# Optimization experiments

Measured on AMD Instinct MI355X. Metric: run time of the kernel, lower is better.

Reference implementation:

```python
import jax, jax.numpy as jnp
import numpy as np

TREE_DEPTH = 8
N_INTERNAL = 2 ** TREE_DEPTH - 1   # 255
N_LEAVES = 2 ** TREE_DEPTH         # 256
N_CLASSES = 100
N_TREES = 16
BATCH = 8192
D_FEAT = 1024
TEMPERATURE = 1.0


def setup_inputs() -> dict:
    key = jax.random.key(0)
    k1, k2, k3, k4, k5 = jax.random.split(key, 5)
    x = jax.random.normal(k1, (BATCH, D_FEAT), dtype=jnp.float32)
    # scale weights ~1/sqrt(D) so split logits are O(1) (avoids sigmoid saturation)
    split_weights = jax.random.normal(k2, (N_TREES, N_INTERNAL, D_FEAT), dtype=jnp.float32) / np.sqrt(D_FEAT)
    split_bias = jax.random.normal(k3, (N_TREES, N_INTERNAL), dtype=jnp.float32)
    leaf_logits = jax.random.normal(k4, (N_TREES, N_LEAVES, N_CLASSES), dtype=jnp.float32)
    tree_weights = jax.random.normal(k5, (N_TREES,), dtype=jnp.float32)
    return {"x": x, "split_weights": split_weights, "split_bias": split_bias,
            "leaf_logits": leaf_logits, "tree_weights": tree_weights}


def reference(x, split_weights, split_bias, leaf_logits, tree_weights):
    # All internal-node split logits in one contraction: [T, B, N_INTERNAL]
    logits = jnp.einsum('bd,tnd->tbn', x, split_weights) + split_bias[:, None, :]
    split_prob = jax.nn.sigmoid(logits / TEMPERATURE)  # P(go right) per heap node
    T, B = split_prob.shape[0], split_prob.shape[1]
    # Level-order path products. Heap layout: level d occupies nodes [2^d-1, 2^(d+1)-2].
    # Child j of a node splits into (left=2j, right=2j+1) at next level -> interleave.
    mu = jnp.ones((T, B, 1), dtype=x.dtype)
    for d in range(TREE_DEPTH):
        start = 2 ** d - 1
        p = split_prob[:, :, start:start + 2 ** d]          # [T, B, 2^d]
        mu = jnp.stack([mu * (1.0 - p), mu * p], axis=-1)   # left, right
        mu = mu.reshape(T, B, 2 ** (d + 1))
    # mu: [T, B, N_LEAVES] leaf reach probabilities, ordering matches leaf_idx
    leaf_dist = jax.nn.softmax(leaf_logits, axis=-1)        # [T, L, C]
    per_tree = jnp.einsum('tbl,tlc->tbc', mu, leaf_dist)    # [T, B, C]
    w = jax.nn.softmax(tree_weights, axis=0)[:, None, None]
    return (per_tree * w).sum(axis=0)                       # [B, C]
```

## Files before the change

kernel.cpp:

```cpp
#include <hip/hip_runtime.h>
#include <hip/hip_fp16.h>

typedef _Float16 f16;
typedef _Float16 f16x4 __attribute__((ext_vector_type(4)));
typedef _Float16 f16x8 __attribute__((ext_vector_type(8)));
typedef float    f32x4 __attribute__((ext_vector_type(4)));

constexpr int TREES = 16;
constexpr int NNODE = 255;
constexpr int NCLS  = 100;
constexpr int NCPAD = 112;
constexpr int NB    = 8192;
constexpr int DF    = 1024;
constexpr int KTOT  = TREES * 256;

constexpr size_t XH_OFF = 0;
constexpr size_t WH_OFF = XH_OFF + (size_t)NB * DF;
constexpr size_t SD_OFF = WH_OFF + (size_t)TREES * 256 * DF;
constexpr size_t BP_OFF = SD_OFF + (size_t)NCPAD * KTOT;
constexpr size_t PT_OFF_F = (BP_OFF + 8192) / 2;

#define WAIT_VMCNT(n) asm volatile("s_waitcnt vmcnt(" #n ")" ::: "memory")
__device__ __forceinline__ void BAR() {
  asm volatile("" ::: "memory");
  __builtin_amdgcn_s_barrier();
  asm volatile("" ::: "memory");
}

__device__ __forceinline__ void gload_lds16(const f16* g, f16* l) {
  __builtin_amdgcn_global_load_lds(
      (const __attribute__((address_space(1))) void*)g,
      (__attribute__((address_space(3))) void*)l, 16, 0, 0);
}

__global__ void prep_all_k(const float* __restrict__ x, const float* __restrict__ w,
                           const float* __restrict__ ll, const float* __restrict__ twin,
                           const float* __restrict__ sb,
                           f16* __restrict__ xh, f16* __restrict__ wh,
                           f16* __restrict__ sdt, float* __restrict__ bp) {
  int bid = blockIdx.x;
  if (bid < 4096) {
    int i = bid * 256 + threadIdx.x;
    const float4* s = (const float4*)x + (size_t)i * 2;
    float4 u = s[0], v = s[1];
    f16x8 h = {(f16)u.x, (f16)u.y, (f16)u.z, (f16)u.w,
               (f16)v.x, (f16)v.y, (f16)v.z, (f16)v.w};
    *((f16x8*)xh + i) = h;
  } else if (bid < 6144) {
    int i = (bid - 4096) * 256 + threadIdx.x;
    int flat = i * 8;
    int t = flat >> 18;
    int r = (flat >> 10) & 255;
    int k = flat & 1023;
    f16x8 h;
    if (r < NNODE) {
      const float4* s = (const float4*)(w + ((size_t)(t * NNODE + r) * DF + k));
      float4 u = s[0], v = s[1];
      h = (f16x8){(f16)u.x, (f16)u.y, (f16)u.z, (f16)u.w,
                  (f16)v.x, (f16)v.y, (f16)v.z, (f16)v.w};
    } else {
      h = (f16x8){(f16)0.f, (f16)0.f, (f16)0.f, (f16)0.f,
                  (f16)0.f, (f16)0.f, (f16)0.f, (f16)0.f};
    }
    *((f16x8*)wh + i) = h;
  } else {
    int wv   = threadIdx.x >> 6;
    int lane = threadIdx.x & 63;
    int id   = (bid - 6144) * 4 + wv;
    int t    = id >> 8;
    int node = id & 255;

    float wm = -1e30f;
#pragma unroll
    for (int i = 0; i < 16; ++i) wm = fmaxf(wm, twin[i]);
    float wsum = 0.f;
#pragma unroll
    for (int i = 0; i < 16; ++i) wsum += __expf(twin[i] - wm);
    float wt = __expf(twin[t] - wm) / wsum;

    const float* rowp = ll + (size_t)id * NCLS;
    float v1 = rowp[lane];
    bool has2 = (lane + 64) < NCLS;
    float v2 = has2 ? rowp[lane + 64] : -1e30f;
    float mx = fmaxf(v1, v2);
#pragma unroll
    for (int m = 32; m; m >>= 1) mx = fmaxf(mx, __shfl_xor(mx, m, 64));
    float e1 = __expf(v1 - mx);
    float e2 = has2 ? __expf(v2 - mx) : 0.f;
    float ss = e1 + e2;
#pragma unroll
    for (int m = 32; m; m >>= 1) ss += __shfl_xor(ss, m, 64);
    float inv = wt / ss;

    sdt[(size_t)lane * KTOT + id] = (f16)(e1 * inv);
    if (lane + 64 < NCPAD)
      sdt[(size_t)(lane + 64) * KTOT + id] = has2 ? (f16)(e2 * inv) : (f16)0.f;
    if (lane == 0) bp[id] = (node < NNODE) ? sb[(size_t)t * NNODE + node] : 0.f;
  }
}

__global__ __launch_bounds__(512, 2) void tree_gemm1(
    const f16* __restrict__ xh, const f16* __restrict__ wh,
    const float* __restrict__ biasp, const f16* __restrict__ sdt,
    float* __restrict__ ptree) {
  __shared__ f16 smem[81920];
  char* smb = (char*)smem;

  const int tid  = threadIdx.x;
  const int lane = tid & 63;
  const int wid  = tid >> 6;
  const int l15  = lane & 15;
  const int lq   = lane >> 4;
  const int wrow = (wid >> 2) * 128;
  const int wcol = (wid & 3) * 64;

  int bid  = blockIdx.x;
  int xcd  = bid & 7;
  int idx  = bid >> 3;
  int t    = (xcd & 1) * 8 + (idx & 7);
  int brow = (xcd >> 1) * 8 + (idx >> 3);

  const f16* xsrc = xh + (size_t)brow * 256 * DF;
  const f16* wsrc = wh + (size_t)t * 256 * DF;

  auto stage_ht = [&](int kt, int cb, int op, int kh) {
    const f16* srcb = (op == 0 ? xsrc : wsrc) + kt * 64 + kh * 32;
    f16* dstb = smem + cb * 32768 + op * 16384 + kh * 8192;
#pragma unroll
    for (int ch = 0; ch < 2; ++ch) {
      int u  = ch * 512 + tid;
      int r0 = ((u >> 2) ^ (u >> 4)) & 1;
      int r1 = (u >> 3) & 1;
      int r2 = (u >> 4) & 1;
      int r  = r0 | (r1 << 1) | (r2 << 2) | ((u >> 5) << 3);
      int cs = ((u ^ r0) & 1) | ((((u >> 1) ^ r1) & 1) << 1);
      gload_lds16(srcb + (size_t)r * DF + cs * 8, dstb + u * 8);
    }
  };

  auto sdt_stage2 = [&](int c) {
#pragma unroll
    for (int ch = 0; ch < 2; ++ch) {
      int q  = c * 1024 + ch * 512 + tid;
      int rr = q >> 5;
      int jj = q & 31;
      gload_lds16(sdt + (size_t)rr * KTOT + t * 256 + ((jj * 8) ^ ((rr & 7) << 3)),
                  smem + q * 8);
    }
  };

  auto ldop = [&](const char* half_base, int row) -> f16x8 {
    return *(const f16x8*)(half_base + ((row * 64 + lq * 16) ^ ((row & 7) << 4)));
  };

  f32x4 acc[8][4];
#pragma unroll
  for (int m = 0; m < 8; ++m)
#pragma unroll
    for (int n = 0; n < 4; ++n) acc[m][n] = (f32x4){0.f, 0.f, 0.f, 0.f};

  stage_ht(0, 0, 0, 0); stage_ht(0, 0, 1, 0);
  stage_ht(0, 0, 0, 1); stage_ht(0, 0, 1, 1);

  for (int kt = 0; kt < 16; ++kt) {
    const char* Acur = smb + (kt & 1) * 65536;
    const char* Bcur = Acur + 32768;
    const int cn = (kt & 1) ^ 1;
    f16x8 af[4], bf[4];

    if (kt < 15) stage_ht(kt + 1, cn, 0, 0); else sdt_stage2(0);
    WAIT_VMCNT(6);
    BAR();
#pragma unroll
    for (int m = 0; m < 4; ++m) af[m] = ldop(Acur, wrow + m * 16 + l15);
#pragma unroll
    for (int n = 0; n < 4; ++n) bf[n] = ldop(Bcur, wcol + n * 16 + l15);
    __builtin_amdgcn_s_setprio(1);
#pragma unroll
    for (int m = 0; m < 4; ++m)
#pragma unroll
      for (int n = 0; n < 4; ++n)
        acc[m][n] = __builtin_amdgcn_mfma_f32_16x16x32_f16(bf[n], af[m], acc[m][n], 0, 0, 0);
    __builtin_amdgcn_s_setprio(0);
    BAR();

#pragma unroll
    for (int m = 0; m < 4; ++m) af[m] = ldop(Acur, wrow + 64 + m * 16 + l15);
    if (kt < 15) stage_ht(kt + 1, cn, 1, 0);
    BAR();
    __builtin_amdgcn_sched_barrier(0);
    __builtin_amdgcn_s_setprio(1);
#pragma unroll
    for (int m = 0; m < 4; ++m)
#pragma unroll
      for (int n = 0; n < 4; ++n)
        acc[m + 4][n] = __builtin_amdgcn_mfma_f32_16x16x32_f16(bf[n], af[m], acc[m + 4][n], 0, 0, 0);
    __builtin_amdgcn_s_setprio(0);
    BAR();

    if (kt < 15) { stage_ht(kt + 1, cn, 0, 1); WAIT_VMCNT(6); }
    else         { sdt_stage2(1);              WAIT_VMCNT(4); }
    BAR();
#pragma unroll
    for (int m = 0; m < 4; ++m) af[m] = ldop(Acur + 16384, wrow + m * 16 + l15);
#pragma unroll
    for (int n = 0; n < 4; ++n) bf[n] = ldop(Bcur + 16384, wcol + n * 16 + l15);
    __builtin_amdgcn_s_setprio(1);
#pragma unroll
    for (int m = 0; m < 4; ++m)
#pragma unroll
      for (int n = 0; n < 4; ++n)
        acc[m][n] = __builtin_amdgcn_mfma_f32_16x16x32_f16(bf[n], af[m], acc[m][n], 0, 0, 0);
    __builtin_amdgcn_s_setprio(0);
    BAR();

#pragma unroll
    for (int m = 0; m < 4; ++m) af[m] = ldop(Acur + 16384, wrow + 64 + m * 16 + l15);
    if (kt < 15) stage_ht(kt + 1, cn, 1, 1);
    BAR();
    __builtin_amdgcn_sched_barrier(0);
    __builtin_amdgcn_s_setprio(1);
#pragma unroll
    for (int m = 0; m < 4; ++m)
#pragma unroll
      for (int n = 0; n < 4; ++n)
        acc[m + 4][n] = __builtin_amdgcn_mfma_f32_16x16x32_f16(bf[n], af[m], acc[m + 4][n], 0, 0, 0);
    __builtin_amdgcn_s_setprio(0);
    BAR();
  }

  char* Sb = smb;
  char* Ub = smb + 32768;
  char* Pb = smb + 98304;

  auto stage_sdt = [&](int c0, int nrows) {
    int nch = nrows * 32;
    for (int q = tid; q < nch; q += 512) {
      int rr = q >> 5;
      int jj = q & 31;
      gload_lds16(sdt + (size_t)(c0 + rr) * KTOT + t * 256 + ((jj * 8) ^ ((rr & 7) << 3)),
                  smem + q * 8);
    }
  };

  f16x4 ph[8][4];
#pragma unroll
  for (int m = 0; m < 8; ++m) {
#pragma unroll
    for (int n = 0; n < 4; ++n) {
      int col = wcol + n * 16 + lq * 4;
      float4 b4 = *(const float4*)(biasp + t * 256 + col);
#pragma unroll
      for (int reg = 0; reg < 4; ++reg) {
        float bv = (reg == 0) ? b4.x : (reg == 1) ? b4.y : (reg == 2) ? b4.z : b4.w;
        float z = acc[m][n][reg] + bv;
        ph[m][n][reg] = (f16)__builtin_amdgcn_rcpf(1.f + __expf(-z));
      }
    }
  }

  for (int h = 0; h < 2; ++h) {
    if ((wid >> 2) == h) {
#pragma unroll
      for (int m = 0; m < 8; ++m) {
#pragma unroll
        for (int n = 0; n < 4; ++n) {
          int r = m * 16 + l15;
          int nodeb = (wcol + n * 16 + lq * 4) * 2;
          *(f16x4*)(Pb + ((r * 512 + nodeb) ^ ((r & 7) << 4))) = ph[m][n];
        }
      }
    }
    __syncthreads();

    {
      int r = tid >> 2;
      int c = tid & 3;
      auto PRs = [&](int node) -> float {
        return (float)*(const f16*)(Pb + ((r * 512 + node * 2) ^ ((r & 7) << 4)));
      };
      auto V8 = [&](int node) -> f16x8 {
        return *(const f16x8*)(Pb + ((r * 512 + node * 2) ^ ((r & 7) << 4)));
      };
      float p0 = PRs(0);
      float p1 = PRs(1 + (c >> 1));
      float pr = ((c >> 1) ? p0 : 1.f - p0) * ((c & 1) ? p1 : 1.f - p1);
      float p2 = PRs(3 + c);
      float cur[64];
      {
        float mp = pr * p2;
        cur[1] = mp; cur[0] = pr - mp;
      }
      {
        float q0 = PRs(7 + 2 * c), q1 = PRs(8 + 2 * c);
        float m1 = cur[1], mp1 = m1 * q1;
        cur[3] = mp1; cur[2] = m1 - mp1;
        float m0 = cur[0], mp0 = m0 * q0;
        cur[1] = mp0; cur[0] = m0 - mp0;
      }
      {
        float q[4];
        q[0] = PRs(15 + 4 * c);
        f16x4 v = *(const f16x4*)(Pb + ((r * 512 + (16 + 4 * c) * 2) ^ ((r & 7) << 4)));
        q[1] = (float)v[0]; q[2] = (float)v[1]; q[3] = (float)v[2];
#pragma unroll
        for (int i = 3; i >= 0; --i) {
          float mv = cur[i], mp = mv * q[i];
          cur[2 * i + 1] = mp; cur[2 * i] = mv - mp;
        }
      }
      {
        float q[8];
        q[0] = PRs(31 + 8 * c);
        f16x8 v = V8(32 + 8 * c);
#pragma unroll
        for (int j = 0; j < 7; ++j) q[j + 1] = (float)v[j];
#pragma unroll
        for (int i = 7; i >= 0; --i) {
          float mv = cur[i], mp = mv * q[i];
          cur[2 * i + 1] = mp; cur[2 * i] = mv - mp;
        }
      }
      {
        float q[16];
        q[0] = PRs(63 + 16 * c);
        f16x8 v0 = V8(64 + 16 * c), v1 = V8(72 + 16 * c);
#pragma unroll
        for (int j = 0; j < 8; ++j) q[j + 1] = (float)v0[j];
#pragma unroll
        for (int j = 0; j < 7; ++j) q[j + 9] = (float)v1[j];
#pragma unroll
        for (int i = 15; i >= 0; --i) {
          float mv = cur[i], mp = mv * q[i];
          cur[2 * i + 1] = mp; cur[2 * i] = mv - mp;
        }
      }
      {
        float q[32];
        q[0] = PRs(127 + 32 * c);
        f16x8 v0 = V8(128 + 32 * c), v1 = V8(136 + 32 * c);
        f16x8 v2 = V8(144 + 32 * c), v3 = V8(152 + 32 * c);
#pragma unroll
        for (int j = 0; j < 8; ++j) q[j + 1]  = (float)v0[j];
#pragma unroll
        for (int j = 0; j < 8; ++j) q[j + 9]  = (float)v1[j];
#pragma unroll
        for (int j = 0; j < 8; ++j) q[j + 17] = (float)v2[j];
#pragma unroll
        for (int j = 0; j < 7; ++j) q[j + 25] = (float)v3[j];
#pragma unroll
        for (int i = 31; i >= 0; --i) {
          float mv = cur[i], mp = mv * q[i];
          cur[2 * i + 1] = mp; cur[2 * i] = mv - mp;
        }
      }
#pragma unroll
      for (int g = 0; g < 8; ++g) {
        f16x8 v;
#pragma unroll
        for (int jj = 0; jj < 8; ++jj) v[jj] = (f16)cur[g * 8 + jj];
        *(f16x8*)(Ub + ((r * 512 + c * 128 + g * 16) ^ ((r & 7) << 4))) = v;
      }
    }
    WAIT_VMCNT(0);
    __syncthreads();

    f32x4 acc2[7];
#pragma unroll
    for (int n = 0; n < 7; ++n) acc2[n] = (f32x4){0.f, 0.f, 0.f, 0.f};
    int arow = wid * 16 + l15;

#pragma unroll
    for (int n = 0; n < 4; ++n) {
#pragma unroll
      for (int s = 0; s < 8; ++s) {
        f16x8 a = *(const f16x8*)(Ub + ((arow * 512 + s * 64 + lq * 16) ^ ((arow & 7) << 4)));
        int br = n * 16 + l15;
        f16x8 b = *(const f16x8*)(Sb + ((br * 512 + s * 64 + lq * 16) ^ ((br & 7) << 4)));
        acc2[n] = __builtin_amdgcn_mfma_f32_16x16x32_f16(a, b, acc2[n], 0, 0, 0);
      }
    }
    __syncthreads();
    stage_sdt(64, 48);
    WAIT_VMCNT(0);
    __syncthreads();
#pragma unroll
    for (int n = 4; n < 7; ++n) {
#pragma unroll
      for (int s = 0; s < 8; ++s) {
        f16x8 a = *(const f16x8*)(Ub + ((arow * 512 + s * 64 + lq * 16) ^ ((arow & 7) << 4)));
        int br = (n - 4) * 16 + l15;
        f16x8 b = *(const f16x8*)(Sb + ((br * 512 + s * 64 + lq * 16) ^ ((br & 7) << 4)));
        acc2[n] = __builtin_amdgcn_mfma_f32_16x16x32_f16(a, b, acc2[n], 0, 0, 0);
      }
    }

    float* pt = ptree + ((size_t)t * NB + brow * 256 + h * 128) * NCLS;
#pragma unroll
    for (int n = 0; n < 7; ++n) {
      int col = n * 16 + l15;
      if (col < NCLS) {
#pragma unroll
        for (int reg = 0; reg < 4; ++reg) {
          int r = wid * 16 + lq * 4 + reg;
          pt[(size_t)r * NCLS + col] = acc2[n][reg];
        }
      }
    }
    if (h == 0) {
      __syncthreads();
      stage_sdt(0, 64);
    }
  }
}

__global__ void reduce_k(const float* __restrict__ pt, float* __restrict__ out) {
  int i = blockIdx.x * 256 + threadIdx.x;
  constexpr size_t STRIDE4 = (size_t)NB * NCLS / 4;
  const float4* p = (const float4*)pt + i;
  float4 s = p[0];
#pragma unroll
  for (int t = 1; t < TREES; ++t) {
    float4 v = p[t * STRIDE4];
    s.x += v.x; s.y += v.y; s.z += v.z; s.w += v.w;
  }
  ((float4*)out)[i] = s;
}

extern "C" void kernel_launch(void* const* d_in, const int* in_sizes, int n_in,
                              void* d_out, int out_size, void* d_ws, size_t ws_size,
                              hipStream_t stream) {
  const float* x  = (const float*)d_in[0];
  const float* sw = (const float*)d_in[1];
  const float* sb = (const float*)d_in[2];
  const float* ll = (const float*)d_in[3];
  const float* tw = (const float*)d_in[4];
  float* out = (float*)d_out;

  f16* ws  = (f16*)d_ws;
  f16* xh  = ws + XH_OFF;
  f16* wh  = ws + WH_OFF;
  f16* sdt = ws + SD_OFF;
  float* biasp = (float*)(ws + BP_OFF);
  float* ptree = (float*)d_ws + PT_OFF_F;

  prep_all_k<<<7168, 256, 0, stream>>>(x, sw, ll, tw, sb, xh, wh, sdt, biasp);
  tree_gemm1<<<512, 512, 0, stream>>>(xh, wh, biasp, sdt, ptree);
  reduce_k<<<(NB * NCLS / 4) / 256, 256, 0, stream>>>(ptree, out);
}
```

Baseline: 199.1 us.

## Merge main GEMM loop into two k-half phases and hoist A fragments in leaf GEMM

The main split-logit GEMM loop is restructured from four sub-phases per k-tile into two. Each phase issues the A and B staging loads together, then loads all eight A fragments and four B fragments and runs 32 MFMAs. This halves the number of barriers and waitcnts per iteration. The second (leaf-distribution) GEMM now loads the A row fragments once into registers and reuses them across both column passes instead of re-reading LDS. The cost is higher register pressure from keeping eight A fragments live, and less interleaving of global loads with compute.

```diff
diff --git a/kernel.cpp b/kernel.cpp
--- a/kernel.cpp
+++ b/kernel.cpp
@@ -123,9 +123,12 @@
   const f16* xsrc = xh + (size_t)brow * 256 * DF;
   const f16* wsrc = wh + (size_t)t * 256 * DF;
 
-  auto stage_ht = [&](int kt, int cb, int op, int kh) {
-    const f16* srcb = (op == 0 ? xsrc : wsrc) + kt * 64 + kh * 32;
-    f16* dstb = smem + cb * 32768 + op * 16384 + kh * 8192;
+  auto stage_AB = [&](int kt, int kh) {
+    int cb = kt & 1;
+    const f16* asrcb = xsrc + kt * 64 + kh * 32;
+    const f16* bsrcb = wsrc + kt * 64 + kh * 32;
+    f16* adst = smem + cb * 32768 + kh * 8192;
+    f16* bdst = adst + 16384;
 #pragma unroll
     for (int ch = 0; ch < 2; ++ch) {
       int u  = ch * 512 + tid;
@@ -134,14 +137,15 @@
       int r2 = (u >> 4) & 1;
       int r  = r0 | (r1 << 1) | (r2 << 2) | ((u >> 5) << 3);
       int cs = ((u ^ r0) & 1) | ((((u >> 1) ^ r1) & 1) << 1);
-      gload_lds16(srcb + (size_t)r * DF + cs * 8, dstb + u * 8);
+      gload_lds16(asrcb + (size_t)r * DF + cs * 8, adst + u * 8);
+      gload_lds16(bsrcb + (size_t)r * DF + cs * 8, bdst + u * 8);
     }
   };
 
-  auto sdt_stage2 = [&](int c) {
-#pragma unroll
-    for (int ch = 0; ch < 2; ++ch) {
-      int q  = c * 1024 + ch * 512 + tid;
+  auto sdt_stage4 = [&]() {
+#pragma unroll
+    for (int ch = 0; ch < 4; ++ch) {
+      int q  = ch * 512 + tid;
       int rr = q >> 5;
       int jj = q & 31;
       gload_lds16(sdt + (size_t)rr * KTOT + t * 256 + ((jj * 8) ^ ((rr & 7) << 3)),
@@ -159,74 +163,35 @@
 #pragma unroll
     for (int n = 0; n < 4; ++n) acc[m][n] = (f32x4){0.f, 0.f, 0.f, 0.f};
 
-  stage_ht(0, 0, 0, 0); stage_ht(0, 0, 1, 0);
-  stage_ht(0, 0, 0, 1); stage_ht(0, 0, 1, 1);
+  stage_AB(0, 0);
+  stage_AB(0, 1);
 
   for (int kt = 0; kt < 16; ++kt) {
     const char* Acur = smb + (kt & 1) * 65536;
     const char* Bcur = Acur + 32768;
-    const int cn = (kt & 1) ^ 1;
-    f16x8 af[4], bf[4];
-
-    if (kt < 15) stage_ht(kt + 1, cn, 0, 0); else sdt_stage2(0);
-    WAIT_VMCNT(6);
-    BAR();
-#pragma unroll
-    for (int m = 0; m < 4; ++m) af[m] = ldop(Acur, wrow + m * 16 + l15);
-#pragma unroll
-    for (int n = 0; n < 4; ++n) bf[n] = ldop(Bcur, wcol + n * 16 + l15);
-    __builtin_amdgcn_s_setprio(1);
-#pragma unroll
-    for (int m = 0; m < 4; ++m)
-#pragma unroll
-      for (int n = 0; n < 4; ++n)
-        acc[m][n] = __builtin_amdgcn_mfma_f32_16x16x32_f16(bf[n], af[m], acc[m][n], 0, 0, 0);
-    __builtin_amdgcn_s_setprio(0);
-    BAR();
-
-#pragma unroll
-    for (int m = 0; m < 4; ++m) af[m] = ldop(Acur, wrow + 64 + m * 16 + l15);
-    if (kt < 15) stage_ht(kt + 1, cn, 1, 0);
-    BAR();
-    __builtin_amdgcn_sched_barrier(0);
-    __builtin_amdgcn_s_setprio(1);
-#pragma unroll
-    for (int m = 0; m < 4; ++m)
-#pragma unroll
-      for (int n = 0; n < 4; ++n)
-        acc[m + 4][n] = __builtin_amdgcn_mfma_f32_16x16x32_f16(bf[n], af[m], acc[m + 4][n], 0, 0, 0);
-    __builtin_amdgcn_s_setprio(0);
-    BAR();
-
-    if (kt < 15) { stage_ht(kt + 1, cn, 0, 1); WAIT_VMCNT(6); }
-    else         { sdt_stage2(1);              WAIT_VMCNT(4); }
-    BAR();
-#pragma unroll
-    for (int m = 0; m < 4; ++m) af[m] = ldop(Acur + 16384, wrow + m * 16 + l15);
-#pragma unroll
-    for (int n = 0; n < 4; ++n) bf[n] = ldop(Bcur + 16384, wcol + n * 16 + l15);
-    __builtin_amdgcn_s_setprio(1);
-#pragma unroll
-    for (int m = 0; m < 4; ++m)
-#pragma unroll
-      for (int n = 0; n < 4; ++n)
-        acc[m][n] = __builtin_amdgcn_mfma_f32_16x16x32_f16(bf[n], af[m], acc[m][n], 0, 0, 0);
-    __builtin_amdgcn_s_setprio(0);
-    BAR();
-
-#pragma unroll
-    for (int m = 0; m < 4; ++m) af[m] = ldop(Acur + 16384, wrow + 64 + m * 16 + l15);
-    if (kt < 15) stage_ht(kt + 1, cn, 1, 1);
-    BAR();
-    __builtin_amdgcn_sched_barrier(0);
-    __builtin_amdgcn_s_setprio(1);
-#pragma unroll
-    for (int m = 0; m < 4; ++m)
-#pragma unroll
-      for (int n = 0; n < 4; ++n)
-        acc[m + 4][n] = __builtin_amdgcn_mfma_f32_16x16x32_f16(bf[n], af[m], acc[m + 4][n], 0, 0, 0);
-    __builtin_amdgcn_s_setprio(0);
-    BAR();
+#pragma unroll
+    for (int kh = 0; kh < 2; ++kh) {
+      if (kt < 15)      stage_AB(kt + 1, kh);
+      else if (kh == 0) sdt_stage4();
+      if (kt < 15 || kh == 0) { WAIT_VMCNT(8); }
+      else                    { WAIT_VMCNT(4); }
+      BAR();
+      const char* Ah = Acur + kh * 16384;
+      const char* Bh = Bcur + kh * 16384;
+      f16x8 af[8], bf[4];
+#pragma unroll
+      for (int m = 0; m < 8; ++m) af[m] = ldop(Ah, wrow + m * 16 + l15);
+#pragma unroll
+      for (int n = 0; n < 4; ++n) bf[n] = ldop(Bh, wcol + n * 16 + l15);
+      __builtin_amdgcn_s_setprio(1);
+#pragma unroll
+      for (int m = 0; m < 8; ++m)
+#pragma unroll
+        for (int n = 0; n < 4; ++n)
+          acc[m][n] = __builtin_amdgcn_mfma_f32_16x16x32_f16(bf[n], af[m], acc[m][n], 0, 0, 0);
+      __builtin_amdgcn_s_setprio(0);
+      BAR();
+    }
   }
 
   char* Sb = smb;
@@ -370,14 +335,18 @@
     for (int n = 0; n < 7; ++n) acc2[n] = (f32x4){0.f, 0.f, 0.f, 0.f};
     int arow = wid * 16 + l15;
 
-#pragma unroll
-    for (int n = 0; n < 4; ++n) {
-#pragma unroll
-      for (int s = 0; s < 8; ++s) {
-        f16x8 a = *(const f16x8*)(Ub + ((arow * 512 + s * 64 + lq * 16) ^ ((arow & 7) << 4)));
+    f16x8 a8[8];
+#pragma unroll
+    for (int s = 0; s < 8; ++s)
+      a8[s] = *(const f16x8*)(Ub + ((arow * 512 + s * 64 + lq * 16) ^ ((arow & 7) << 4)));
+
+#pragma unroll
+    for (int s = 0; s < 8; ++s) {
+#pragma unroll
+      for (int n = 0; n < 4; ++n) {
         int br = n * 16 + l15;
         f16x8 b = *(const f16x8*)(Sb + ((br * 512 + s * 64 + lq * 16) ^ ((br & 7) << 4)));
-        acc2[n] = __builtin_amdgcn_mfma_f32_16x16x32_f16(a, b, acc2[n], 0, 0, 0);
+        acc2[n] = __builtin_amdgcn_mfma_f32_16x16x32_f16(a8[s], b, acc2[n], 0, 0, 0);
       }
     }
     __syncthreads();
@@ -385,13 +354,12 @@
     WAIT_VMCNT(0);
     __syncthreads();
 #pragma unroll
-    for (int n = 4; n < 7; ++n) {
-#pragma unroll
-      for (int s = 0; s < 8; ++s) {
-        f16x8 a = *(const f16x8*)(Ub + ((arow * 512 + s * 64 + lq * 16) ^ ((arow & 7) << 4)));
+    for (int s = 0; s < 8; ++s) {
+#pragma unroll
+      for (int n = 4; n < 7; ++n) {
         int br = (n - 4) * 16 + l15;
         f16x8 b = *(const f16x8*)(Sb + ((br * 512 + s * 64 + lq * 16) ^ ((br & 7) << 4)));
-        acc2[n] = __builtin_amdgcn_mfma_f32_16x16x32_f16(a, b, acc2[n], 0, 0, 0);
+        acc2[n] = __builtin_amdgcn_mfma_f32_16x16x32_f16(a8[s], b, acc2[n], 0, 0, 0);
       }
     }
 
```

After: 218.5 us. +9.7%, slower.
